# Kernel tuning notes

Measured on AMD Instinct MI355X. Metric: run time of the kernel, lower is better.

## Reference

```python
import jax, jax.numpy as jnp
import numpy as np

R_SOFTPLUS_0 = 1.442695041  # 1/softplus(0) = 1/ln(2)
NEG_INF = -1e9


def setup_inputs() -> dict:
    key = jax.random.key(0)
    ks = jax.random.split(key, 6)
    B, L, E, H = 16, 1024, 512, 8
    Dh = E // H
    return {
        "x": jax.random.normal(ks[0], (B, L, E), jnp.float32),
        "in_proj_weight": jax.random.normal(ks[1], (3 * E, E), jnp.float32) * (E ** -0.5),
        "in_proj_bias": jax.random.normal(ks[2], (3 * E,), jnp.float32) * 0.02,
        "out_proj_weight": jax.random.normal(ks[3], (E, E), jnp.float32) * (E ** -0.5),
        "out_proj_bias": jax.random.normal(ks[4], (E,), jnp.float32) * 0.02,
        "qs_scale": jnp.zeros((Dh,), jnp.float32),  # init.zeros in QueryScaler
        "key_padding_mask": jnp.zeros((B, L), jnp.bool_),  # True = ignore key
    }


def reference(x, in_proj_weight, in_proj_bias, out_proj_weight, out_proj_bias,
              qs_scale, key_padding_mask):
    B, L, E = x.shape
    Dh = qs_scale.shape[0]
    H = E // Dh
    # packed in-projection: q,k,v = x @ W^T + b, split along last dim
    qkv = jnp.einsum("ble,fe->blf", x, in_proj_weight) + in_proj_bias
    q, k, v = jnp.split(qkv, 3, axis=-1)
    q = q.reshape(B, L, H, Dh)
    k = k.reshape(B, L, H, Dh)
    v = v.reshape(B, L, H, Dh)
    # QueryScaler: per-head-dim learned softplus scale on projected q
    q = q * (R_SOFTPLUS_0 * jax.nn.softplus(qs_scale))
    # scaled dot-product attention
    scores = jnp.einsum("blhd,bshd->bhls", q, k) / jnp.sqrt(jnp.asarray(Dh, q.dtype))
    scores = jnp.where(key_padding_mask[:, None, None, :], NEG_INF, scores)
    probs = jax.nn.softmax(scores, axis=-1)
    out = jnp.einsum("bhls,bshd->blhd", probs, v).reshape(B, L, E)
    # output projection
    return jnp.einsum("ble,fe->blf", out, out_proj_weight) + out_proj_bias
```

## Files before the change

### kernel.cpp

```cpp
#include <hip/hip_runtime.h>
#include <hip/hip_bf16.h>
#include <math.h>

#define B_ 16
#define L_ 1024
#define E_ 512
#define H_ 8
#define DH 64

typedef unsigned short u16;
typedef __attribute__((ext_vector_type(8))) short bf16x8;
typedef __attribute__((ext_vector_type(8))) unsigned short u16x8;
typedef __attribute__((ext_vector_type(4))) float f32x4;
typedef __attribute__((ext_vector_type(16))) float f32x16;

#define MFMA16(A, B, C) __builtin_amdgcn_mfma_f32_16x16x32_bf16(A, B, C, 0, 0, 0)
#define MFMA32(A, B, C) __builtin_amdgcn_mfma_f32_32x32x16_bf16(A, B, C, 0, 0, 0)

#if __has_builtin(__builtin_amdgcn_exp2f)
#define EXP2(x) __builtin_amdgcn_exp2f(x)
#else
#define EXP2(x) exp2f(x)
#endif

__device__ inline u16 f2b(float x) {
    __hip_bfloat16 h = __float2bfloat16(x);
    u16 u; __builtin_memcpy(&u, &h, 2); return u;
}

__device__ inline unsigned int cvt_pk_bf16(float a, float b) {
    unsigned int r;
    asm("v_cvt_pk_bf16_f32 %0, %1, %2" : "=v"(r) : "v"(a), "v"(b));
    return r;
}

__global__ __launch_bounds__(256) void cvt_bf16(
    const float* __restrict__ x, const float* __restrict__ wi,
    const float* __restrict__ wo, const float* __restrict__ qs_scale,
    u16* __restrict__ xb, u16* __restrict__ wib, u16* __restrict__ wob,
    float* __restrict__ qscale)
{
    if (blockIdx.x == 0 && threadIdx.x < DH) {
        float s = qs_scale[threadIdx.x];
        float sp = (s > 20.f) ? s : log1pf(expf(s));
        qscale[threadIdx.x] = 1.442695041f * sp * 0.125f * 1.442695041f;
    }
    int i = blockIdx.x * 256 + threadIdx.x;
    const float* src; u16* dst; size_t off;
    if (i < 1048576)      { src = x;  dst = xb;  off = (size_t)i * 8; }
    else if (i < 1146880) { src = wi; dst = wib; off = (size_t)(i - 1048576) * 8; }
    else                  { src = wo; dst = wob; off = (size_t)(i - 1146880) * 8; }
    float4 a = *(const float4*)(src + off);
    float4 b = *(const float4*)(src + off + 4);
    u16x8 r;
    r[0] = f2b(a.x); r[1] = f2b(a.y); r[2] = f2b(a.z); r[3] = f2b(a.w);
    r[4] = f2b(b.x); r[5] = f2b(b.y); r[6] = f2b(b.z); r[7] = f2b(b.w);
    *(u16x8*)(dst + off) = r;
}

template<int MODE>
__global__ __launch_bounds__(256) void gemm_bf16(
    const u16* __restrict__ A, const u16* __restrict__ W,
    const float* __restrict__ bias, const float* __restrict__ qscale,
    float* __restrict__ Dout, u16* __restrict__ Qb, u16* __restrict__ Kb,
    u16* __restrict__ Vtb)
{
    __shared__ u16 sA[2][4096];
    __shared__ u16 sB[2][4096];
    const int tid = threadIdx.x;
    const int m0 = blockIdx.x * 128;
    const int n0 = blockIdx.y * 128;
    const int wid = tid >> 6, lane = tid & 63;
    const int g = lane >> 4, c = lane & 15;
    const int wr = wid >> 1, wc = wid & 1;

    const int arow = tid >> 2;
    const int swg = (arow & 3) ^ ((arow >> 2) & 3);
    const int ch = (tid & 3) ^ swg;
    const u16* Asrc = A + (size_t)(m0 + arow) * 512 + ch * 8;
    const u16* Bsrc = W + (size_t)(n0 + arow) * 512 + ch * 8;

    auto stage = [&](int nbuf, int ks) {
        const int k0 = ks * 32;
        __builtin_amdgcn_global_load_lds(
            (const __attribute__((address_space(1))) unsigned int*)(Asrc + k0),
            (__attribute__((address_space(3))) unsigned int*)&sA[nbuf][wid * 512], 16, 0, 0);
        __builtin_amdgcn_global_load_lds(
            (const __attribute__((address_space(1))) unsigned int*)(Asrc + (size_t)64 * 512 + k0),
            (__attribute__((address_space(3))) unsigned int*)&sA[nbuf][2048 + wid * 512], 16, 0, 0);
        __builtin_amdgcn_global_load_lds(
            (const __attribute__((address_space(1))) unsigned int*)(Bsrc + k0),
            (__attribute__((address_space(3))) unsigned int*)&sB[nbuf][wid * 512], 16, 0, 0);
        __builtin_amdgcn_global_load_lds(
            (const __attribute__((address_space(1))) unsigned int*)(Bsrc + (size_t)64 * 512 + k0),
            (__attribute__((address_space(3))) unsigned int*)&sB[nbuf][2048 + wid * 512], 16, 0, 0);
    };

    f32x4 acc[4][4];
    #pragma unroll
    for (int m = 0; m < 4; m++)
        #pragma unroll
        for (int n = 0; n < 4; n++) acc[m][n] = (f32x4){0.f, 0.f, 0.f, 0.f};

    const int swr = (c & 3) ^ ((c >> 2) & 3);
    const int chA = (g ^ swr) * 8;

    stage(0, 0);
    #pragma unroll 1
    for (int ks = 0; ks < 16; ks++) {
        const int cur = ks & 1;
        asm volatile("s_waitcnt vmcnt(0) lgkmcnt(0)" ::: "memory");
        __syncthreads();
        if (ks < 15) stage(cur ^ 1, ks + 1);

        bf16x8 af[4], bfr[4];
        #pragma unroll
        for (int m = 0; m < 4; m++)
            af[m] = *(const bf16x8*)&sA[cur][(wr * 64 + m * 16 + c) * 32 + chA];
        #pragma unroll
        for (int n = 0; n < 4; n++)
            bfr[n] = *(const bf16x8*)&sB[cur][(wc * 64 + n * 16 + c) * 32 + chA];
        #pragma unroll
        for (int m = 0; m < 4; m++)
            #pragma unroll
            for (int n = 0; n < 4; n++)
                acc[m][n] = MFMA16(af[m], bfr[n], acc[m][n]);
    }

    #pragma unroll
    for (int m = 0; m < 4; m++) {
        int rbase = m0 + wr * 64 + m * 16 + 4 * g;
        #pragma unroll
        for (int n = 0; n < 4; n++) {
            int f = n0 + wc * 64 + n * 16 + c;
            f32x4 v = acc[m][n];
            float bv = bias[f];
            if (MODE == 1) {
                #pragma unroll
                for (int reg = 0; reg < 4; reg++)
                    Dout[(size_t)(rbase + reg) * E_ + f] = v[reg] + bv;
            } else {
                int part = f >> 9, w = f & 511, h = w >> 6, d = w & 63;
                int bb = rbase >> 10;
                int l0 = rbase & 1023;
                size_t bh = (size_t)(bb * H_ + h);
                if (part == 0) {
                    float qs = qscale[d];
                    #pragma unroll
                    for (int reg = 0; reg < 4; reg++)
                        Qb[(bh * L_ + l0 + reg) * DH + d] = f2b((v[reg] + bv) * qs);
                } else if (part == 1) {
                    #pragma unroll
                    for (int reg = 0; reg < 4; reg++)
                        Kb[(bh * L_ + l0 + reg) * DH + d] = f2b(v[reg] + bv);
                } else {
                    ushort4 pk;
                    pk.x = f2b(v[0] + bv); pk.y = f2b(v[1] + bv);
                    pk.z = f2b(v[2] + bv); pk.w = f2b(v[3] + bv);
                    *(ushort4*)(Vtb + (bh * DH + d) * L_ + l0) = pk;
                }
            }
        }
    }
}

__global__ __launch_bounds__(256, 4) void attn_mfma(
    const u16* __restrict__ Q, const u16* __restrict__ K,
    const u16* __restrict__ Vt, const unsigned char* __restrict__ mask,
    u16* __restrict__ O)
{
    __shared__ u16 Kbuf[3][2048];
    __shared__ u16 Vbuf[3][2048];

    const int bid = blockIdx.x;
    const int w = (bid & 7) * 128 + (bid >> 3);
    const int bh = w >> 3;
    const int blk = w & 7;
    const int tid = threadIdx.x;
    const int wid = tid >> 6;
    const int q0 = blk * 128 + wid * 32;
    const int b = bh >> 3;
    const int h = bh & (H_ - 1);

    const int lane = tid & 63;
    const int c = lane & 31;
    const int hi = lane >> 5;

    const u16* Qp = Q + ((size_t)bh * L_ + q0) * DH;
    const u16* Kp = K + (size_t)bh * L_ * DH;
    const u16* Vp = Vt + (size_t)bh * DH * L_;
    const unsigned char* mp = mask + (size_t)b * L_;

    const int krow = tid >> 3, kch = (tid & 7) ^ (krow & 7);
    const int vrow = tid >> 2, vch = (tid & 3) ^ ((vrow & 3) ^ ((vrow >> 2) & 3));
    const u16* Kg = Kp + (size_t)krow * DH + kch * 8;
    const u16* Vg = Vp + (size_t)vrow * L_ + vch * 8;

    auto stage = [&](int nbuf, int kt) {
        __builtin_amdgcn_global_load_lds(
            (const __attribute__((address_space(1))) unsigned int*)(Kg + (size_t)kt * DH),
            (__attribute__((address_space(3))) unsigned int*)&Kbuf[nbuf][wid * 512],
            16, 0, 0);
        __builtin_amdgcn_global_load_lds(
            (const __attribute__((address_space(1))) unsigned int*)(Vg + kt),
            (__attribute__((address_space(3))) unsigned int*)&Vbuf[nbuf][wid * 512],
            16, 0, 0);
    };

    unsigned int mor = 0;
    {
        const unsigned int* mp32 = (const unsigned int*)mp;
        #pragma unroll
        for (int i = 0; i < 4; i++) mor |= mp32[lane + i * 64];
    }
    const bool anyMask = (__ballot(mor != 0) != 0ULL);

    bf16x8 qf[4];
    #pragma unroll
    for (int s2 = 0; s2 < 4; s2++)
        qf[s2] = *(const bf16x8*)(Qp + c * DH + s2 * 16 + hi * 8);

    stage(0, 0);
    stage(1, 32);

    f32x16 oacc0 = {}, oacc1 = {};
    float mrun = -INFINITY, lrun = 0.f;

    int kslot[4];
    #pragma unroll
    for (int s2 = 0; s2 < 4; s2++)
        kslot[s2] = (c * 8 + (((2 * s2 + hi)) ^ (c & 7))) * 8;
    const int swzv = (c & 3) ^ ((c >> 2) & 3);
    int vslot[2][2];
    #pragma unroll
    for (int dt = 0; dt < 2; dt++)
        #pragma unroll
        for (int s = 0; s < 2; s++)
            vslot[dt][s] = ((dt * 32 + c) * 4 + (((2 * s + hi)) ^ swzv)) * 8;

    #pragma unroll 1
    for (int t = 0; t < 32; ++t) {
        const int cur = t % 3;
        const int kt = t * 32;
        if (t < 31) { asm volatile("s_waitcnt vmcnt(2) lgkmcnt(0)" ::: "memory"); }
        else        { asm volatile("s_waitcnt vmcnt(0) lgkmcnt(0)" ::: "memory"); }
        __builtin_amdgcn_s_barrier();
        asm volatile("" ::: "memory");

        bf16x8 kf[4];
        #pragma unroll
        for (int s2 = 0; s2 < 4; s2++)
            kf[s2] = *(const bf16x8*)&Kbuf[cur][kslot[s2]];
        bf16x8 vf[2][2];
        #pragma unroll
        for (int dt = 0; dt < 2; dt++)
            #pragma unroll
            for (int s = 0; s < 2; s++)
                vf[dt][s] = *(const bf16x8*)&Vbuf[cur][vslot[dt][s]];

        if (t < 30) stage((t + 2) % 3, kt + 64);

        f32x16 st = {};
        #pragma unroll
        for (int s2 = 0; s2 < 4; s2++)
            st = MFMA32(kf[s2], qf[s2], st);

        if (anyMask) {
            #pragma unroll
            for (int r = 0; r < 16; r++) {
                int key = kt + (r & 3) + 8 * (r >> 2) + 4 * hi;
                if (mp[key]) st[r] = -1e9f;
            }
        }

        float m01 = fmaxf(st[0], st[1]),  m23 = fmaxf(st[2], st[3]);
        float m45 = fmaxf(st[4], st[5]),  m67 = fmaxf(st[6], st[7]);
        float m89 = fmaxf(st[8], st[9]),  mab = fmaxf(st[10], st[11]);
        float mcd = fmaxf(st[12], st[13]), mef = fmaxf(st[14], st[15]);
        float tm = fmaxf(fmaxf(fmaxf(m01, m23), fmaxf(m45, m67)),
                         fmaxf(fmaxf(m89, mab), fmaxf(mcd, mef)));
        tm = fmaxf(tm, __shfl_xor(tm, 32));

        if (!__all(tm <= mrun + 8.f)) {
            float mnew = fmaxf(mrun, tm);
            float corr = EXP2(mrun - mnew);
            lrun *= corr;
            #pragma unroll
            for (int r = 0; r < 16; r++) {
                int row = (r & 3) + 8 * (r >> 2) + 4 * hi;
                float cr = __shfl(corr, row);
                oacc0[r] *= cr;
                oacc1[r] *= cr;
            }
            mrun = mnew;
        }

        float p[16];
        #pragma unroll
        for (int r = 0; r < 16; r++) p[r] = EXP2(st[r] - mrun);
        float s01 = (p[0] + p[1]) + (p[2] + p[3]);
        float s23 = (p[4] + p[5]) + (p[6] + p[7]);
        float s45 = (p[8] + p[9]) + (p[10] + p[11]);
        float s67 = (p[12] + p[13]) + (p[14] + p[15]);
        float ls = (s01 + s23) + (s45 + s67);
        ls += __shfl_xor(ls, 32);
        lrun += ls;

        unsigned int x0 = cvt_pk_bf16(p[0],  p[1]);
        unsigned int x1 = cvt_pk_bf16(p[2],  p[3]);
        unsigned int y0 = cvt_pk_bf16(p[4],  p[5]);
        unsigned int y1 = cvt_pk_bf16(p[6],  p[7]);
        unsigned int x2 = cvt_pk_bf16(p[8],  p[9]);
        unsigned int x3 = cvt_pk_bf16(p[10], p[11]);
        unsigned int y2 = cvt_pk_bf16(p[12], p[13]);
        unsigned int y3 = cvt_pk_bf16(p[14], p[15]);
        asm volatile("v_permlane32_swap_b32 %0, %1" : "+v"(x0), "+v"(y0));
        asm volatile("v_permlane32_swap_b32 %0, %1" : "+v"(x1), "+v"(y1));
        asm volatile("v_permlane32_swap_b32 %0, %1" : "+v"(x2), "+v"(y2));
        asm volatile("v_permlane32_swap_b32 %0, %1" : "+v"(x3), "+v"(y3));
        union { unsigned int u[4]; bf16x8 v; } pk0u, pk1u;
        pk0u.u[0] = x0; pk0u.u[1] = x1; pk0u.u[2] = y0; pk0u.u[3] = y1;
        pk1u.u[0] = x2; pk1u.u[1] = x3; pk1u.u[2] = y2; pk1u.u[3] = y3;
        bf16x8 pa0 = pk0u.v;
        bf16x8 pa1 = pk1u.v;

        oacc0 = MFMA32(pa0, vf[0][0], oacc0);
        oacc0 = MFMA32(pa1, vf[0][1], oacc0);
        oacc1 = MFMA32(pa0, vf[1][0], oacc1);
        oacc1 = MFMA32(pa1, vf[1][1], oacc1);
    }

    #pragma unroll
    for (int r = 0; r < 16; r++) {
        int row = (r & 3) + 8 * (r >> 2) + 4 * hi;
        float lq = __shfl(lrun, row);
        float inv = 1.f / lq;
        size_t base = ((size_t)(b * L_ + q0 + row)) * E_ + h * DH + c;
        O[base] = f2b(oacc0[r] * inv);
        O[base + 32] = f2b(oacc1[r] * inv);
    }
}

extern "C" void kernel_launch(void* const* d_in, const int* in_sizes, int n_in,
                              void* d_out, int out_size, void* d_ws, size_t ws_size,
                              hipStream_t stream) {
    const float* x     = (const float*)d_in[0];
    const float* w_in  = (const float*)d_in[1];
    const float* b_in  = (const float*)d_in[2];
    const float* w_out = (const float*)d_in[3];
    const float* b_out = (const float*)d_in[4];
    const float* qs    = (const float*)d_in[5];
    const unsigned char* mask = (const unsigned char*)d_in[6];
    float* out = (float*)d_out;

    char* base = (char*)d_ws;
    const size_t NELEM = (size_t)B_ * L_ * E_;
    float* qscale = (float*)base;
    u16* xb  = (u16*)(base + 256);
    u16* wib = xb + NELEM;
    u16* wob = wib + 786432;
    u16* Qb  = wob + 262144;
    u16* Kb  = Qb + NELEM;
    u16* Vtb = Kb + NELEM;
    u16* Ob  = Vtb + NELEM;

    cvt_bf16<<<4608, 256, 0, stream>>>(x, w_in, w_out, qs, xb, wib, wob, qscale);
    gemm_bf16<0><<<dim3(128, 12), 256, 0, stream>>>(
        xb, wib, b_in, qscale, nullptr, Qb, Kb, Vtb);
    attn_mfma<<<dim3(1024), 256, 0, stream>>>(Qb, Kb, Vtb, mask, Ob);
    gemm_bf16<1><<<dim3(128, 4), 256, 0, stream>>>(
        Ob, wob, b_out, nullptr, out, nullptr, nullptr, nullptr);
}
```

Before: 123.6 us.

## Process 64-key tiles per iteration with double buffering in attention kernel

The attention main loop now handles 64 keys per iteration instead of 32, halving iteration count and barrier/softmax-bookkeeping overhead. Shared-memory staging moves from a triple-buffered 32-key pipeline to a double-buffered 64-key one, with a single full wait and __syncthreads per iteration. The V layout switches to a 64-element row swizzle, and exp2 is emitted as raw v_exp_f32. The trade-offs are shallower prefetch depth (only one tile ahead, with a full vmcnt(0) drain) and higher register pressure from two score tiles.

Result: no change. 124.3 us (+0.6%).

```diff
diff --git a/kernel.cpp b/kernel.cpp
--- a/kernel.cpp
+++ b/kernel.cpp
@@ -17,15 +17,13 @@
 #define MFMA16(A, B, C) __builtin_amdgcn_mfma_f32_16x16x32_bf16(A, B, C, 0, 0, 0)
 #define MFMA32(A, B, C) __builtin_amdgcn_mfma_f32_32x32x16_bf16(A, B, C, 0, 0, 0)
 
-#if __has_builtin(__builtin_amdgcn_exp2f)
-#define EXP2(x) __builtin_amdgcn_exp2f(x)
-#else
-#define EXP2(x) exp2f(x)
-#endif
-
 __device__ inline u16 f2b(float x) {
     __hip_bfloat16 h = __float2bfloat16(x);
     u16 u; __builtin_memcpy(&u, &h, 2); return u;
+}
+
+__device__ inline float exp2_hw(float x) {
+    float r; asm("v_exp_f32 %0, %1" : "=v"(r) : "v"(x)); return r;
 }
 
 __device__ inline unsigned int cvt_pk_bf16(float a, float b) {
@@ -169,8 +167,8 @@
     const u16* __restrict__ Vt, const unsigned char* __restrict__ mask,
     u16* __restrict__ O)
 {
-    __shared__ u16 Kbuf[3][2048];
-    __shared__ u16 Vbuf[3][2048];
+    __shared__ u16 Kbuf[2][4096];
+    __shared__ u16 Vbuf[2][4096];
 
     const int bid = blockIdx.x;
     const int w = (bid & 7) * 128 + (bid >> 3);
@@ -191,10 +189,10 @@
     const u16* Vp = Vt + (size_t)bh * DH * L_;
     const unsigned char* mp = mask + (size_t)b * L_;
 
-    const int krow = tid >> 3, kch = (tid & 7) ^ (krow & 7);
-    const int vrow = tid >> 2, vch = (tid & 3) ^ ((vrow & 3) ^ ((vrow >> 2) & 3));
-    const u16* Kg = Kp + (size_t)krow * DH + kch * 8;
-    const u16* Vg = Vp + (size_t)vrow * L_ + vch * 8;
+    const int srow = tid >> 3;
+    const int sch = (tid & 7) ^ (srow & 7);
+    const u16* Kg = Kp + (size_t)srow * DH + sch * 8;
+    const u16* Vg = Vp + (size_t)srow * L_ + sch * 8;
 
     auto stage = [&](int nbuf, int kt) {
         __builtin_amdgcn_global_load_lds(
@@ -202,9 +200,17 @@
             (__attribute__((address_space(3))) unsigned int*)&Kbuf[nbuf][wid * 512],
             16, 0, 0);
         __builtin_amdgcn_global_load_lds(
+            (const __attribute__((address_space(1))) unsigned int*)(Kg + (size_t)(kt + 32) * DH),
+            (__attribute__((address_space(3))) unsigned int*)&Kbuf[nbuf][2048 + wid * 512],
+            16, 0, 0);
+        __builtin_amdgcn_global_load_lds(
             (const __attribute__((address_space(1))) unsigned int*)(Vg + kt),
             (__attribute__((address_space(3))) unsigned int*)&Vbuf[nbuf][wid * 512],
             16, 0, 0);
+        __builtin_amdgcn_global_load_lds(
+            (const __attribute__((address_space(1))) unsigned int*)(Vg + (size_t)32 * L_ + kt),
+            (__attribute__((address_space(3))) unsigned int*)&Vbuf[nbuf][2048 + wid * 512],
+            16, 0, 0);
     };
 
     unsigned int mor = 0;
@@ -221,7 +227,6 @@
         qf[s2] = *(const bf16x8*)(Qp + c * DH + s2 * 16 + hi * 8);
 
     stage(0, 0);
-    stage(1, 32);
 
     f32x16 oacc0 = {}, oacc1 = {};
     float mrun = -INFINITY, lrun = 0.f;
@@ -229,61 +234,53 @@
     int kslot[4];
     #pragma unroll
     for (int s2 = 0; s2 < 4; s2++)
-        kslot[s2] = (c * 8 + (((2 * s2 + hi)) ^ (c & 7))) * 8;
-    const int swzv = (c & 3) ^ ((c >> 2) & 3);
-    int vslot[2][2];
-    #pragma unroll
-    for (int dt = 0; dt < 2; dt++)
-        #pragma unroll
-        for (int s = 0; s < 2; s++)
-            vslot[dt][s] = ((dt * 32 + c) * 4 + (((2 * s + hi)) ^ swzv)) * 8;
-
-    #pragma unroll 1
-    for (int t = 0; t < 32; ++t) {
-        const int cur = t % 3;
-        const int kt = t * 32;
-        if (t < 31) { asm volatile("s_waitcnt vmcnt(2) lgkmcnt(0)" ::: "memory"); }
-        else        { asm volatile("s_waitcnt vmcnt(0) lgkmcnt(0)" ::: "memory"); }
-        __builtin_amdgcn_s_barrier();
-        asm volatile("" ::: "memory");
-
-        bf16x8 kf[4];
-        #pragma unroll
-        for (int s2 = 0; s2 < 4; s2++)
-            kf[s2] = *(const bf16x8*)&Kbuf[cur][kslot[s2]];
-        bf16x8 vf[2][2];
+        kslot[s2] = (c * 8 + ((2 * s2 + hi) ^ (c & 7))) * 8;
+    int vslot[2][2][2];
+    #pragma unroll
+    for (int hf = 0; hf < 2; hf++)
         #pragma unroll
         for (int dt = 0; dt < 2; dt++)
             #pragma unroll
             for (int s = 0; s < 2; s++)
-                vf[dt][s] = *(const bf16x8*)&Vbuf[cur][vslot[dt][s]];
-
-        if (t < 30) stage((t + 2) % 3, kt + 64);
-
-        f32x16 st = {};
-        #pragma unroll
-        for (int s2 = 0; s2 < 4; s2++)
-            st = MFMA32(kf[s2], qf[s2], st);
+                vslot[hf][dt][s] = ((dt * 32 + c) * 8 + ((hf * 4 + 2 * s + hi) ^ (c & 7))) * 8;
+
+    #pragma unroll 1
+    for (int t = 0; t < 16; ++t) {
+        const int cur = t & 1;
+        const int kt = t * 64;
+        asm volatile("s_waitcnt vmcnt(0) lgkmcnt(0)" ::: "memory");
+        __syncthreads();
+        if (t < 15) stage(cur ^ 1, kt + 64);
+
+        f32x16 stA = {}, stB = {};
+        #pragma unroll
+        for (int s2 = 0; s2 < 4; s2++) {
+            bf16x8 kfa = *(const bf16x8*)&Kbuf[cur][kslot[s2]];
+            stA = MFMA32(kfa, qf[s2], stA);
+        }
+        #pragma unroll
+        for (int s2 = 0; s2 < 4; s2++) {
+            bf16x8 kfb = *(const bf16x8*)&Kbuf[cur][kslot[s2] + 2048];
+            stB = MFMA32(kfb, qf[s2], stB);
+        }
 
         if (anyMask) {
             #pragma unroll
             for (int r = 0; r < 16; r++) {
                 int key = kt + (r & 3) + 8 * (r >> 2) + 4 * hi;
-                if (mp[key]) st[r] = -1e9f;
+                if (mp[key])      stA[r] = -1e9f;
+                if (mp[key + 32]) stB[r] = -1e9f;
             }
         }
 
-        float m01 = fmaxf(st[0], st[1]),  m23 = fmaxf(st[2], st[3]);
-        float m45 = fmaxf(st[4], st[5]),  m67 = fmaxf(st[6], st[7]);
-        float m89 = fmaxf(st[8], st[9]),  mab = fmaxf(st[10], st[11]);
-        float mcd = fmaxf(st[12], st[13]), mef = fmaxf(st[14], st[15]);
-        float tm = fmaxf(fmaxf(fmaxf(m01, m23), fmaxf(m45, m67)),
-                         fmaxf(fmaxf(m89, mab), fmaxf(mcd, mef)));
-        tm = fmaxf(tm, __shfl_xor(tm, 32));
-
-        if (!__all(tm <= mrun + 8.f)) {
-            float mnew = fmaxf(mrun, tm);
-            float corr = EXP2(mrun - mnew);
+        float tmax = fmaxf(stA[0], stB[0]);
+        #pragma unroll
+        for (int r = 1; r < 16; r++) tmax = fmaxf(tmax, fmaxf(stA[r], stB[r]));
+        tmax = fmaxf(tmax, __shfl_xor(tmax, 32));
+
+        if (!__all(tmax <= mrun + 8.f)) {
+            float mnew = fmaxf(mrun, tmax);
+            float corr = exp2_hw(mrun - mnew);
             lrun *= corr;
             #pragma unroll
             for (int r = 0; r < 16; r++) {
@@ -295,39 +292,68 @@
             mrun = mnew;
         }
 
-        float p[16];
-        #pragma unroll
-        for (int r = 0; r < 16; r++) p[r] = EXP2(st[r] - mrun);
-        float s01 = (p[0] + p[1]) + (p[2] + p[3]);
-        float s23 = (p[4] + p[5]) + (p[6] + p[7]);
-        float s45 = (p[8] + p[9]) + (p[10] + p[11]);
-        float s67 = (p[12] + p[13]) + (p[14] + p[15]);
-        float ls = (s01 + s23) + (s45 + s67);
+        float pA[16], pB[16];
+        #pragma unroll
+        for (int r = 0; r < 16; r++) {
+            pA[r] = exp2_hw(stA[r] - mrun);
+            pB[r] = exp2_hw(stB[r] - mrun);
+        }
+        float ls = 0.f;
+        #pragma unroll
+        for (int r = 0; r < 16; r++) ls += pA[r] + pB[r];
         ls += __shfl_xor(ls, 32);
         lrun += ls;
 
-        unsigned int x0 = cvt_pk_bf16(p[0],  p[1]);
-        unsigned int x1 = cvt_pk_bf16(p[2],  p[3]);
-        unsigned int y0 = cvt_pk_bf16(p[4],  p[5]);
-        unsigned int y1 = cvt_pk_bf16(p[6],  p[7]);
-        unsigned int x2 = cvt_pk_bf16(p[8],  p[9]);
-        unsigned int x3 = cvt_pk_bf16(p[10], p[11]);
-        unsigned int y2 = cvt_pk_bf16(p[12], p[13]);
-        unsigned int y3 = cvt_pk_bf16(p[14], p[15]);
-        asm volatile("v_permlane32_swap_b32 %0, %1" : "+v"(x0), "+v"(y0));
-        asm volatile("v_permlane32_swap_b32 %0, %1" : "+v"(x1), "+v"(y1));
-        asm volatile("v_permlane32_swap_b32 %0, %1" : "+v"(x2), "+v"(y2));
-        asm volatile("v_permlane32_swap_b32 %0, %1" : "+v"(x3), "+v"(y3));
-        union { unsigned int u[4]; bf16x8 v; } pk0u, pk1u;
-        pk0u.u[0] = x0; pk0u.u[1] = x1; pk0u.u[2] = y0; pk0u.u[3] = y1;
-        pk1u.u[0] = x2; pk1u.u[1] = x3; pk1u.u[2] = y2; pk1u.u[3] = y3;
-        bf16x8 pa0 = pk0u.v;
-        bf16x8 pa1 = pk1u.v;
-
-        oacc0 = MFMA32(pa0, vf[0][0], oacc0);
-        oacc0 = MFMA32(pa1, vf[0][1], oacc0);
-        oacc1 = MFMA32(pa0, vf[1][0], oacc1);
-        oacc1 = MFMA32(pa1, vf[1][1], oacc1);
+        {
+            unsigned int x0 = cvt_pk_bf16(pA[0],  pA[1]);
+            unsigned int x1 = cvt_pk_bf16(pA[2],  pA[3]);
+            unsigned int y0 = cvt_pk_bf16(pA[4],  pA[5]);
+            unsigned int y1 = cvt_pk_bf16(pA[6],  pA[7]);
+            unsigned int x2 = cvt_pk_bf16(pA[8],  pA[9]);
+            unsigned int x3 = cvt_pk_bf16(pA[10], pA[11]);
+            unsigned int y2 = cvt_pk_bf16(pA[12], pA[13]);
+            unsigned int y3 = cvt_pk_bf16(pA[14], pA[15]);
+            asm volatile("v_permlane32_swap_b32 %0, %1" : "+v"(x0), "+v"(y0));
+            asm volatile("v_permlane32_swap_b32 %0, %1" : "+v"(x1), "+v"(y1));
+            asm volatile("v_permlane32_swap_b32 %0, %1" : "+v"(x2), "+v"(y2));
+            asm volatile("v_permlane32_swap_b32 %0, %1" : "+v"(x3), "+v"(y3));
+            union { unsigned int u[4]; bf16x8 v; } p0u, p1u;
+            p0u.u[0] = x0; p0u.u[1] = x1; p0u.u[2] = y0; p0u.u[3] = y1;
+            p1u.u[0] = x2; p1u.u[1] = x3; p1u.u[2] = y2; p1u.u[3] = y3;
+            bf16x8 vA00 = *(const bf16x8*)&Vbuf[cur][vslot[0][0][0]];
+            bf16x8 vA01 = *(const bf16x8*)&Vbuf[cur][vslot[0][0][1]];
+            bf16x8 vA10 = *(const bf16x8*)&Vbuf[cur][vslot[0][1][0]];
+            bf16x8 vA11 = *(const bf16x8*)&Vbuf[cur][vslot[0][1][1]];
+            oacc0 = MFMA32(p0u.v, vA00, oacc0);
+            oacc0 = MFMA32(p1u.v, vA01, oacc0);
+            oacc1 = MFMA32(p0u.v, vA10, oacc1);
+            oacc1 = MFMA32(p1u.v, vA11, oacc1);
+        }
+        {
+            unsigned int x0 = cvt_pk_bf16(pB[0],  pB[1]);
+            unsigned int x1 = cvt_pk_bf16(pB[2],  pB[3]);
+            unsigned int y0 = cvt_pk_bf16(pB[4],  pB[5]);
+            unsigned int y1 = cvt_pk_bf16(pB[6],  pB[7]);
+            unsigned int x2 = cvt_pk_bf16(pB[8],  pB[9]);
+            unsigned int x3 = cvt_pk_bf16(pB[10], pB[11]);
+            unsigned int y2 = cvt_pk_bf16(pB[12], pB[13]);
+            unsigned int y3 = cvt_pk_bf16(pB[14], pB[15]);
+            asm volatile("v_permlane32_swap_b32 %0, %1" : "+v"(x0), "+v"(y0));
+            asm volatile("v_permlane32_swap_b32 %0, %1" : "+v"(x1), "+v"(y1));
+            asm volatile("v_permlane32_swap_b32 %0, %1" : "+v"(x2), "+v"(y2));
+            asm volatile("v_permlane32_swap_b32 %0, %1" : "+v"(x3), "+v"(y3));
+            union { unsigned int u[4]; bf16x8 v; } p0u, p1u;
+            p0u.u[0] = x0; p0u.u[1] = x1; p0u.u[2] = y0; p0u.u[3] = y1;
+            p1u.u[0] = x2; p1u.u[1] = x3; p1u.u[2] = y2; p1u.u[3] = y3;
+            bf16x8 vB00 = *(const bf16x8*)&Vbuf[cur][vslot[1][0][0]];
+            bf16x8 vB01 = *(const bf16x8*)&Vbuf[cur][vslot[1][0][1]];
+            bf16x8 vB10 = *(const bf16x8*)&Vbuf[cur][vslot[1][1][0]];
+            bf16x8 vB11 = *(const bf16x8*)&Vbuf[cur][vslot[1][1][1]];
+            oacc0 = MFMA32(p0u.v, vB00, oacc0);
+            oacc0 = MFMA32(p1u.v, vB01, oacc0);
+            oacc1 = MFMA32(p0u.v, vB10, oacc1);
+            oacc1 = MFMA32(p1u.v, vB11, oacc1);
+        }
     }
 
     #pragma unroll
```
